# Optimization experiments

Measured on AMD Instinct MI355X. Metric: run time of the kernel, lower is better.

The kernel has to match this reference:

```python
import jax, jax.numpy as jnp
import numpy as np

N_HEADS = 16

def setup_inputs() -> dict:
    key = jax.random.key(0)
    ks = jax.random.split(key, 5)
    d = 2048
    s = 0.02
    return {
        "x": jax.random.normal(ks[0], (1, 2048, d), dtype=jnp.float32),
        "Wq": jax.random.normal(ks[1], (d, d), dtype=jnp.float32) * s,
        "bq": jnp.zeros((d,), jnp.float32),
        "Wk": jax.random.normal(ks[2], (d, d), dtype=jnp.float32) * s,
        "bk": jnp.zeros((d,), jnp.float32),
        "Wv": jax.random.normal(ks[3], (d, d), dtype=jnp.float32) * s,
        "bv": jnp.zeros((d,), jnp.float32),
        "Wo": jax.random.normal(ks[4], (d, d), dtype=jnp.float32) * s,
        "bo": jnp.zeros((d,), jnp.float32),
    }

def reference(x, Wq, bq, Wk, bk, Wv, bv, Wo, bo):
    B, S, D = x.shape
    H = N_HEADS
    dk = D // H
    # QKV projections -> [B, H, S, dk]
    def proj(W, b):
        return (x @ W + b).reshape(B, S, H, dk).transpose(0, 2, 1, 3)
    q, k, v = proj(Wq, bq), proj(Wk, bk), proj(Wv, bv)
    scores = jnp.einsum('bhqd,bhkd->bhqk', q, k) / jnp.sqrt(jnp.float32(dk))
    # _apply_sliding_window_attention: block-reshaped tril == plain causal mask
    causal = jnp.tril(jnp.ones((S, S), dtype=bool))
    scores = jnp.where(causal, scores, -jnp.inf)
    probs = jax.nn.softmax(scores, axis=-1)
    out = jnp.einsum('bhqk,bhkd->bhqd', probs, v)  # [B,H,S,dk]
    out = out.transpose(0, 2, 1, 3).reshape(B, S, D)
    return out @ Wo + bo
```

## Files before the change

### kernel.cpp

```cpp
#include <hip/hip_runtime.h>
#include <hip/hip_bf16.h>
#include <stdint.h>

typedef unsigned short u16;
typedef __attribute__((ext_vector_type(8))) __bf16 bf16x8;
typedef __attribute__((ext_vector_type(4))) float f32x4;

#define LOG2E 1.4426950408889634f

__device__ __forceinline__ float bf2f(u16 u) {
  union { uint32_t u; float f; } v; v.u = ((uint32_t)u) << 16;
  return v.f;
}

__device__ __forceinline__ uint32_t pk2(float a, float b) {
  union { __hip_bfloat162 h; uint32_t u; } x;
  x.h = __float22bfloat162_rn(make_float2(a, b));
  return x.u;
}

__device__ __forceinline__ void gl_lds16(const void* g, void* l) {
  __builtin_amdgcn_global_load_lds((const __attribute__((address_space(1))) void*)g,
                                   (__attribute__((address_space(3))) void*)l,
                                   16, 0, 0);
}

__device__ __forceinline__ f32x4 mfma16(bf16x8 a, bf16x8 b, f32x4 c) {
  return __builtin_amdgcn_mfma_f32_16x16x32_bf16(a, b, c, 0, 0, 0);
}

__global__ void cvt_bf16(const float* __restrict__ src, u16* __restrict__ dst) {
  int i = (blockIdx.x * 256 + threadIdx.x) * 4;
  float4 f = *(const float4*)(src + i);
  uint2 o;
  o.x = pk2(f.x, f.y);
  o.y = pk2(f.z, f.w);
  *(uint2*)(dst + i) = o;
}

__global__ void transpose_cvt(const float* __restrict__ W0, const float* __restrict__ W1,
                              const float* __restrict__ W2, const float* __restrict__ W3,
                              u16* __restrict__ out) {
  __shared__ float tile[64][65];
  int z = blockIdx.z;
  const float* W = (z == 0) ? W0 : (z == 1) ? W1 : (z == 2) ? W2 : W3;
  u16* dst = out + (size_t)z * 2048 * 2048;
  int k0 = blockIdx.y * 64, n0 = blockIdx.x * 64;
  int lx = threadIdx.x & 63, ly = threadIdx.x >> 6;
#pragma unroll
  for (int p = 0; p < 16; ++p) {
    int row = p * 4 + ly;
    tile[row][lx] = W[(size_t)(k0 + row) * 2048 + n0 + lx];
  }
  __syncthreads();
  int kc = threadIdx.x & 7;
  int rbase = threadIdx.x >> 3;
#pragma unroll
  for (int p = 0; p < 2; ++p) {
    int n = rbase + p * 32;
    uint4 o;
    o.x = pk2(tile[kc * 8 + 0][n], tile[kc * 8 + 1][n]);
    o.y = pk2(tile[kc * 8 + 2][n], tile[kc * 8 + 3][n]);
    o.z = pk2(tile[kc * 8 + 4][n], tile[kc * 8 + 5][n]);
    o.w = pk2(tile[kc * 8 + 6][n], tile[kc * 8 + 7][n]);
    *(uint4*)(dst + (size_t)(n0 + n) * 2048 + k0 + kc * 8) = o;
  }
}

__launch_bounds__(256, 2)
__global__ void gemm_bt(const u16* __restrict__ A, const u16* __restrict__ Bt,
                        const float* __restrict__ b0, const float* __restrict__ b1,
                        const float* __restrict__ b2,
                        u16* __restrict__ outQ, u16* __restrict__ outK,
                        u16* __restrict__ outVT) {
  extern __shared__ char smem[];
  u16* As = (u16*)smem;
  u16* Bs = (u16*)(smem + 16384);
  const int K = 2048;
  const int tid = threadIdx.x;
  const int lane = tid & 63, wid = tid >> 6;
  const int c = lane & 15, q = lane >> 4;
  const int wm = wid >> 1, wn = wid & 1;
  const int tm = blockIdx.y, tn = blockIdx.x;
  const size_t Abase = (size_t)tm * 128 * K;
  const size_t Bbase = (size_t)tn * 128 * K;

  f32x4 acc[4][4] = {};

  for (int kt = 0; kt < K / 64; ++kt) {
#pragma unroll
    for (int t = 0; t < 4; ++t) {
      int slot = wid * 256 + t * 64 + lane;
      int row = slot >> 3, cs = slot & 7;
      int cc = cs ^ (row & 7);
      const u16* ga = A + Abase + (size_t)row * K + kt * 64 + cc * 8;
      gl_lds16(ga, (char*)As + (size_t)(wid * 256 + t * 64) * 16);
      const u16* gb = Bt + Bbase + (size_t)row * K + kt * 64 + cc * 8;
      gl_lds16(gb, (char*)Bs + (size_t)(wid * 256 + t * 64) * 16);
    }
    __syncthreads();
#pragma unroll
    for (int kc = 0; kc < 2; ++kc) {
      bf16x8 af[4], bfr[4];
#pragma unroll
      for (int i = 0; i < 4; ++i) {
        int rowa = wm * 64 + i * 16 + c;
        int cha = ((kc << 2) | q) ^ (rowa & 7);
        af[i] = *(const bf16x8*)((const char*)As + rowa * 128 + cha * 16);
        int rowb = wn * 64 + i * 16 + c;
        int chb = ((kc << 2) | q) ^ (rowb & 7);
        bfr[i] = *(const bf16x8*)((const char*)Bs + rowb * 128 + chb * 16);
      }
#pragma unroll
      for (int i = 0; i < 4; ++i)
#pragma unroll
        for (int j = 0; j < 4; ++j)
          acc[i][j] = mfma16(af[i], bfr[j], acc[i][j]);
    }
    __syncthreads();
  }

  int proj = tn >> 4;
  int h = tn & 15;
  const float* bias = (proj == 0) ? b0 : (proj == 1) ? b1 : b2;
  if (proj < 2) {
    u16* out = (proj == 0) ? outQ : outK;
    float scale = (proj == 0) ? 0.08838834764831845f : 1.0f;
#pragma unroll
    for (int i = 0; i < 4; ++i) {
      int s0 = tm * 128 + wm * 64 + i * 16 + q * 4;
#pragma unroll
      for (int j = 0; j < 4; ++j) {
        int d = wn * 64 + j * 16 + c;
        float bv = bias[h * 128 + d];
        uint32_t p01 = pk2((acc[i][j][0] + bv) * scale, (acc[i][j][1] + bv) * scale);
        uint32_t p23 = pk2((acc[i][j][2] + bv) * scale, (acc[i][j][3] + bv) * scale);
        u16* o = out + ((size_t)h * 2048 + s0) * 128 + d;
        o[0]   = (u16)p01;
        o[128] = (u16)(p01 >> 16);
        o[256] = (u16)p23;
        o[384] = (u16)(p23 >> 16);
      }
    }
  } else {
    u16* Cs = (u16*)smem;
#pragma unroll
    for (int i = 0; i < 4; ++i) {
      int sl = wm * 64 + i * 16 + q * 4;
#pragma unroll
      for (int j = 0; j < 4; ++j) {
        int dl = wn * 64 + j * 16 + c;
        float bv = bias[h * 128 + dl];
        uint2 pk;
        pk.x = pk2(acc[i][j][0] + bv, acc[i][j][1] + bv);
        pk.y = pk2(acc[i][j][2] + bv, acc[i][j][3] + bv);
        *(uint2*)(Cs + dl * 136 + sl) = pk;
      }
    }
    __syncthreads();
#pragma unroll
    for (int rr = 0; rr < 8; ++rr) {
      int d = rr * 16 + (tid >> 4);
      int sc = (tid & 15) * 8;
      uint4 vv = *(const uint4*)(Cs + d * 136 + sc);
      *(uint4*)(outVT + ((size_t)(h * 128 + d)) * 2048 + tm * 128 + sc) = vv;
    }
  }
}

__launch_bounds__(256, 2)
__global__ void gemm_op(const u16* __restrict__ A, const u16* __restrict__ Bt,
                        const float* __restrict__ bias, float* __restrict__ out) {
  extern __shared__ char smem[];
  u16* As = (u16*)smem;
  u16* Bs = (u16*)(smem + 16384);
  const int K = 2048;
  const int tid = threadIdx.x;
  const int lane = tid & 63, wid = tid >> 6;
  const int c = lane & 15, q = lane >> 4;
  const int wm = wid >> 1, wn = wid & 1;
  const int tm = blockIdx.y, tn = blockIdx.x;
  const size_t Abase = (size_t)tm * 128 * K;
  const size_t Bbase = (size_t)tn * 64 * K;

  f32x4 acc[4][2] = {};

  for (int kt = 0; kt < K / 64; ++kt) {
#pragma unroll
    for (int t = 0; t < 4; ++t) {
      int slot = wid * 256 + t * 64 + lane;
      int row = slot >> 3, cs = slot & 7;
      int cc = cs ^ (row & 7);
      gl_lds16(A + Abase + (size_t)row * K + kt * 64 + cc * 8,
               (char*)As + (size_t)(wid * 256 + t * 64) * 16);
    }
#pragma unroll
    for (int t = 0; t < 2; ++t) {
      int slot = wid * 128 + t * 64 + lane;
      int row = slot >> 3, cs = slot & 7;
      int cc = cs ^ (row & 7);
      gl_lds16(Bt + Bbase + (size_t)row * K + kt * 64 + cc * 8,
               (char*)Bs + (size_t)(wid * 128 + t * 64) * 16);
    }
    __syncthreads();
#pragma unroll
    for (int kc = 0; kc < 2; ++kc) {
      bf16x8 af[4], bfr[2];
#pragma unroll
      for (int i = 0; i < 4; ++i) {
        int rowa = wm * 64 + i * 16 + c;
        int cha = ((kc << 2) | q) ^ (rowa & 7);
        af[i] = *(const bf16x8*)((const char*)As + rowa * 128 + cha * 16);
      }
#pragma unroll
      for (int j = 0; j < 2; ++j) {
        int rowb = wn * 32 + j * 16 + c;
        int chb = ((kc << 2) | q) ^ (rowb & 7);
        bfr[j] = *(const bf16x8*)((const char*)Bs + rowb * 128 + chb * 16);
      }
#pragma unroll
      for (int i = 0; i < 4; ++i)
#pragma unroll
        for (int j = 0; j < 2; ++j)
          acc[i][j] = mfma16(af[i], bfr[j], acc[i][j]);
    }
    __syncthreads();
  }

#pragma unroll
  for (int i = 0; i < 4; ++i) {
    int rowg = tm * 128 + wm * 64 + i * 16 + q * 4;
#pragma unroll
    for (int j = 0; j < 2; ++j) {
      int colg = tn * 64 + wn * 32 + j * 16 + c;
      float bv = bias[colg];
#pragma unroll
      for (int r = 0; r < 4; ++r)
        out[(size_t)(rowg + r) * 2048 + colg] = acc[i][j][r] + bv;
    }
  }
}

__launch_bounds__(256, 2)
__global__ void attn_kernel(const u16* __restrict__ Qb, const u16* __restrict__ Kb,
                            const u16* __restrict__ Vt,
                            u16* __restrict__ Opb, float* __restrict__ lpb) {
  extern __shared__ char smem[];
  u16* Ks = (u16*)smem;
  u16* Vs = (u16*)(smem + 16384);
  u16* Ps = (u16*)(smem + 32768);
  int b = blockIdx.x;
  int split, qt, h;
  if (b < 256) { split = 0; qt = b >> 4; h = b & 15; }
  else { split = 1; int idx = b - 256; qt = 15 - (idx >> 4); h = idx & 15; }
  u16* Op = Opb + (size_t)split * 4194304;
  float* lp = lpb + (size_t)split * 32768;
  const int ktBase = split ? (qt + 1) : 0;
  const int ntiles = qt + 1;

  const int tid = threadIdx.x, lane = tid & 63, wid = tid >> 6;
  const int c = lane & 15, q = lane >> 4;

  bf16x8 qf[2][4];
#pragma unroll
  for (int i = 0; i < 2; ++i) {
    int s = qt * 128 + wid * 32 + i * 16 + c;
    const u16* qrow = Qb + ((size_t)h * 2048 + s) * 128;
#pragma unroll
    for (int kc = 0; kc < 4; ++kc)
      qf[i][kc] = *(const bf16x8*)(qrow + kc * 32 + q * 8);
  }

  f32x4 oacc[2][8] = {};
  float lst[2][4] = {};

  for (int tt = 0; tt < ntiles; ++tt) {
    const int kt = ktBase + tt;
    if (tt) __syncthreads();
#pragma unroll
    for (int t = 0; t < 4; ++t) {
      int slot = (wid * 4 + t) * 64 + lane;
      int rowk = slot >> 4, csk = slot & 15;
      int cck = csk ^ (rowk & 7);
      const u16* gk = Kb + ((size_t)h * 2048 + kt * 64 + rowk) * 128 + cck * 8;
      gl_lds16(gk, (char*)Ks + (size_t)((wid * 4 + t) * 64) * 16);
      int rowv = slot >> 3, csv = slot & 7;
      int ccv = csv ^ (rowv & 7);
      const u16* gv = Vt + ((size_t)(h * 128 + rowv)) * 2048 + kt * 64 + ccv * 8;
      gl_lds16(gv, (char*)Vs + (size_t)((wid * 4 + t) * 64) * 16);
    }
    __syncthreads();

    f32x4 sacc[2][4] = {};
#pragma unroll
    for (int kc = 0; kc < 4; ++kc) {
      bf16x8 bfr[4];
#pragma unroll
      for (int j = 0; j < 4; ++j) {
        int row = j * 16 + c;
        int ch = ((kc << 2) | q) ^ (row & 7);
        bfr[j] = *(const bf16x8*)((const char*)Ks + row * 256 + ch * 16);
      }
#pragma unroll
      for (int i = 0; i < 2; ++i)
#pragma unroll
        for (int j = 0; j < 4; ++j)
          sacc[i][j] = mfma16(qf[i][kc], bfr[j], sacc[i][j]);
    }

    if (kt >= 2 * qt) {
#pragma unroll
      for (int i = 0; i < 2; ++i)
#pragma unroll
        for (int j = 0; j < 4; ++j) {
          int key = kt * 64 + j * 16 + c;
#pragma unroll
          for (int r = 0; r < 4; ++r) {
            int qrow = qt * 128 + wid * 32 + i * 16 + q * 4 + r;
            if (key > qrow) sacc[i][j][r] = -1e30f;
          }
        }
    }

#pragma unroll
    for (int i = 0; i < 2; ++i)
#pragma unroll
      for (int j = 0; j < 4; ++j)
#pragma unroll
        for (int r = 0; r < 4; ++r) {
          float p = __builtin_amdgcn_exp2f(sacc[i][j][r] * LOG2E);
          sacc[i][j][r] = p;
          lst[i][r] += p;
        }

#pragma unroll
    for (int i = 0; i < 2; ++i)
#pragma unroll
      for (int j = 0; j < 4; ++j) {
        uint32_t p01 = pk2(sacc[i][j][0], sacc[i][j][1]);
        uint32_t p23 = pk2(sacc[i][j][2], sacc[i][j][3]);
        u16* pp = Ps + wid * 2304 + (i * 16 + q * 4) * 72 + j * 16 + c;
        pp[0]   = (u16)p01;
        pp[72]  = (u16)(p01 >> 16);
        pp[144] = (u16)p23;
        pp[216] = (u16)(p23 >> 16);
      }

#pragma unroll
    for (int kc = 0; kc < 2; ++kc) {
      bf16x8 af[2], bv[8];
#pragma unroll
      for (int i = 0; i < 2; ++i)
        af[i] = *(const bf16x8*)((const char*)Ps + wid * 4608 + (i * 16 + c) * 144 +
                                 kc * 64 + q * 16);
#pragma unroll
      for (int jo = 0; jo < 8; ++jo) {
        int row = jo * 16 + c;
        int ch = ((kc << 2) | q) ^ (row & 7);
        bv[jo] = *(const bf16x8*)((const char*)Vs + row * 128 + ch * 16);
      }
#pragma unroll
      for (int i = 0; i < 2; ++i)
#pragma unroll
        for (int jo = 0; jo < 8; ++jo)
          oacc[i][jo] = mfma16(bv[jo], af[i], oacc[i][jo]);
    }
  }

#pragma unroll
  for (int i = 0; i < 2; ++i)
#pragma unroll
    for (int r = 0; r < 4; ++r) {
      float l = lst[i][r];
      l += __shfl_xor(l, 1);
      l += __shfl_xor(l, 2);
      l += __shfl_xor(l, 4);
      l += __shfl_xor(l, 8);
      if (c == 0)
        lp[(size_t)h * 2048 + qt * 128 + wid * 32 + i * 16 + q * 4 + r] = l;
    }
#pragma unroll
  for (int i = 0; i < 2; ++i) {
    int s = qt * 128 + wid * 32 + i * 16 + c;
#pragma unroll
    for (int jo = 0; jo < 8; ++jo) {
      uint2 o;
      o.x = pk2(oacc[i][jo][0], oacc[i][jo][1]);
      o.y = pk2(oacc[i][jo][2], oacc[i][jo][3]);
      *(uint2*)(Op + ((size_t)h * 2048 + s) * 128 + jo * 16 + q * 4) = o;
    }
  }
}

__global__ void attn_combine(const u16* __restrict__ Opb, const float* __restrict__ lpb,
                             u16* __restrict__ AO) {
  int g = blockIdx.x * 256 + threadIdx.x;
  int row = g >> 4;
  int dd = (g & 15) * 8;
  int h = row >> 11, s = row & 2047;
  float inv = 1.0f / (lpb[row] + lpb[row + 32768]);
  uint4 a = *(const uint4*)(Opb + (size_t)row * 128 + dd);
  uint4 bb = *(const uint4*)(Opb + 4194304 + (size_t)row * 128 + dd);
  const u16* pa = (const u16*)&a;
  const u16* pb = (const u16*)&bb;
  uint4 res;
  uint32_t* pr = (uint32_t*)&res;
#pragma unroll
  for (int t = 0; t < 4; ++t)
    pr[t] = pk2((bf2f(pa[2 * t]) + bf2f(pb[2 * t])) * inv,
                (bf2f(pa[2 * t + 1]) + bf2f(pb[2 * t + 1])) * inv);
  *(uint4*)(AO + (size_t)s * 2048 + h * 128 + dd) = res;
}

extern "C" void kernel_launch(void* const* d_in, const int* in_sizes, int n_in,
                              void* d_out, int out_size, void* d_ws, size_t ws_size,
                              hipStream_t stream) {
  const float* x  = (const float*)d_in[0];
  const float* Wq = (const float*)d_in[1];
  const float* bq = (const float*)d_in[2];
  const float* Wk = (const float*)d_in[3];
  const float* bk = (const float*)d_in[4];
  const float* Wv = (const float*)d_in[5];
  const float* bv = (const float*)d_in[6];
  const float* Wo = (const float*)d_in[7];
  const float* bo = (const float*)d_in[8];

  char* ws = (char*)d_ws;
  u16* xb = (u16*)(ws);
  u16* wt = (u16*)(ws + (size_t)8  * 1048576);
  u16* Qb = (u16*)(ws + (size_t)40 * 1048576);
  u16* Kb = (u16*)(ws + (size_t)48 * 1048576);
  u16* Vt = (u16*)(ws + (size_t)56 * 1048576);
  u16* AO = (u16*)(ws + (size_t)64 * 1048576);
  u16* Opb = (u16*)(ws);
  float* lpb = (float*)d_out;

  cvt_bf16<<<4096, 256, 0, stream>>>(x, xb);
  transpose_cvt<<<dim3(32, 32, 4), 256, 0, stream>>>(Wq, Wk, Wv, Wo, wt);
  gemm_bt<<<dim3(48, 16), 256, 34816, stream>>>(xb, wt, bq, bk, bv, Qb, Kb, Vt);
  attn_kernel<<<512, 256, 51200, stream>>>(Qb, Kb, Vt, Opb, lpb);
  attn_combine<<<2048, 256, 0, stream>>>(Opb, lpb, AO);
  gemm_op<<<dim3(32, 16), 256, 24576, stream>>>(AO, wt + (size_t)3 * 2048 * 2048,
                                                bo, (float*)d_out);
}
```

Before: 260.7 us.

## Double-buffer K/V tiles in attention with async prefetch and swizzled P buffer

Measured after the change: 256.9 us. Within noise of the previous version (-1.4%).

```diff
diff --git a/kernel.cpp b/kernel.cpp
--- a/kernel.cpp
+++ b/kernel.cpp
@@ -27,6 +27,12 @@
 
 __device__ __forceinline__ f32x4 mfma16(bf16x8 a, bf16x8 b, f32x4 c) {
   return __builtin_amdgcn_mfma_f32_16x16x32_bf16(a, b, c, 0, 0, 0);
+}
+
+__device__ __forceinline__ void bar() {
+  asm volatile("" ::: "memory");
+  __builtin_amdgcn_s_barrier();
+  asm volatile("" ::: "memory");
 }
 
 __global__ void cvt_bf16(const float* __restrict__ src, u16* __restrict__ dst) {
@@ -246,9 +252,6 @@
                             const u16* __restrict__ Vt,
                             u16* __restrict__ Opb, float* __restrict__ lpb) {
   extern __shared__ char smem[];
-  u16* Ks = (u16*)smem;
-  u16* Vs = (u16*)(smem + 16384);
-  u16* Ps = (u16*)(smem + 32768);
   int b = blockIdx.x;
   int split, qt, h;
   if (b < 256) { split = 0; qt = b >> 4; h = b & 15; }
@@ -274,24 +277,43 @@
   f32x4 oacc[2][8] = {};
   float lst[2][4] = {};
 
-  for (int tt = 0; tt < ntiles; ++tt) {
-    const int kt = ktBase + tt;
-    if (tt) __syncthreads();
+  auto STAGE = [&](int kt, int buf) {
+    char* Kd = smem + buf * 32768;
+    char* Vd = smem + buf * 32768 + 16384;
 #pragma unroll
     for (int t = 0; t < 4; ++t) {
       int slot = (wid * 4 + t) * 64 + lane;
       int rowk = slot >> 4, csk = slot & 15;
       int cck = csk ^ (rowk & 7);
       const u16* gk = Kb + ((size_t)h * 2048 + kt * 64 + rowk) * 128 + cck * 8;
-      gl_lds16(gk, (char*)Ks + (size_t)((wid * 4 + t) * 64) * 16);
+      gl_lds16(gk, Kd + (size_t)((wid * 4 + t) * 64) * 16);
       int rowv = slot >> 3, csv = slot & 7;
       int ccv = csv ^ (rowv & 7);
       const u16* gv = Vt + ((size_t)(h * 128 + rowv)) * 2048 + kt * 64 + ccv * 8;
-      gl_lds16(gv, (char*)Vs + (size_t)((wid * 4 + t) * 64) * 16);
-    }
-    __syncthreads();
+      gl_lds16(gv, Vd + (size_t)((wid * 4 + t) * 64) * 16);
+    }
+  };
+
+  STAGE(ktBase, 0);
+  int cur = 0;
+
+  for (int tt = 0; tt < ntiles; ++tt) {
+    const int kt = ktBase + tt;
+    if (tt + 1 < ntiles) {
+      STAGE(kt + 1, cur ^ 1);
+      __builtin_amdgcn_sched_barrier(0);
+      asm volatile("s_waitcnt vmcnt(8)" ::: "memory");
+    } else {
+      asm volatile("s_waitcnt vmcnt(0)" ::: "memory");
+    }
+    __builtin_amdgcn_sched_barrier(0);
+    bar();
+
+    const char* Ksb = smem + cur * 32768;
+    const char* Vsb = smem + cur * 32768 + 16384;
 
     f32x4 sacc[2][4] = {};
+    __builtin_amdgcn_s_setprio(1);
 #pragma unroll
     for (int kc = 0; kc < 4; ++kc) {
       bf16x8 bfr[4];
@@ -299,7 +321,7 @@
       for (int j = 0; j < 4; ++j) {
         int row = j * 16 + c;
         int ch = ((kc << 2) | q) ^ (row & 7);
-        bfr[j] = *(const bf16x8*)((const char*)Ks + row * 256 + ch * 16);
+        bfr[j] = *(const bf16x8*)(Ksb + row * 256 + ch * 16);
       }
 #pragma unroll
       for (int i = 0; i < 2; ++i)
@@ -307,6 +329,8 @@
         for (int j = 0; j < 4; ++j)
           sacc[i][j] = mfma16(qf[i][kc], bfr[j], sacc[i][j]);
     }
+    __builtin_amdgcn_s_setprio(0);
+    bar();
 
     if (kt >= 2 * qt) {
 #pragma unroll
@@ -333,31 +357,36 @@
           lst[i][r] += p;
         }
 
+    char* Pw = smem + cur * 32768 + wid * 4096;
 #pragma unroll
     for (int i = 0; i < 2; ++i)
 #pragma unroll
       for (int j = 0; j < 4; ++j) {
         uint32_t p01 = pk2(sacc[i][j][0], sacc[i][j][1]);
         uint32_t p23 = pk2(sacc[i][j][2], sacc[i][j][3]);
-        u16* pp = Ps + wid * 2304 + (i * 16 + q * 4) * 72 + j * 16 + c;
-        pp[0]   = (u16)p01;
-        pp[72]  = (u16)(p01 >> 16);
-        pp[144] = (u16)p23;
-        pp[216] = (u16)(p23 >> 16);
-      }
-
+        int cb = (j << 1) | (c >> 3);
+        int r0 = i * 16 + q * 4;
+        int wb = (c & 7) << 1;
+        *(u16*)(Pw + (r0 + 0) * 128 + ((cb ^ ((r0 + 0) & 7)) << 4) + wb) = (u16)p01;
+        *(u16*)(Pw + (r0 + 1) * 128 + ((cb ^ ((r0 + 1) & 7)) << 4) + wb) = (u16)(p01 >> 16);
+        *(u16*)(Pw + (r0 + 2) * 128 + ((cb ^ ((r0 + 2) & 7)) << 4) + wb) = (u16)p23;
+        *(u16*)(Pw + (r0 + 3) * 128 + ((cb ^ ((r0 + 3) & 7)) << 4) + wb) = (u16)(p23 >> 16);
+      }
+
+    __builtin_amdgcn_s_setprio(1);
 #pragma unroll
     for (int kc = 0; kc < 2; ++kc) {
       bf16x8 af[2], bv[8];
 #pragma unroll
-      for (int i = 0; i < 2; ++i)
-        af[i] = *(const bf16x8*)((const char*)Ps + wid * 4608 + (i * 16 + c) * 144 +
-                                 kc * 64 + q * 16);
+      for (int i = 0; i < 2; ++i) {
+        int prow = i * 16 + c;
+        af[i] = *(const bf16x8*)(Pw + prow * 128 + ((((kc << 2) | q) ^ (prow & 7)) << 4));
+      }
 #pragma unroll
       for (int jo = 0; jo < 8; ++jo) {
         int row = jo * 16 + c;
         int ch = ((kc << 2) | q) ^ (row & 7);
-        bv[jo] = *(const bf16x8*)((const char*)Vs + row * 128 + ch * 16);
+        bv[jo] = *(const bf16x8*)(Vsb + row * 128 + ch * 16);
       }
 #pragma unroll
       for (int i = 0; i < 2; ++i)
@@ -365,6 +394,9 @@
         for (int jo = 0; jo < 8; ++jo)
           oacc[i][jo] = mfma16(bv[jo], af[i], oacc[i][jo]);
     }
+    __builtin_amdgcn_s_setprio(0);
+    bar();
+    cur ^= 1;
   }
 
 #pragma unroll
@@ -438,7 +470,7 @@
   cvt_bf16<<<4096, 256, 0, stream>>>(x, xb);
   transpose_cvt<<<dim3(32, 32, 4), 256, 0, stream>>>(Wq, Wk, Wv, Wo, wt);
   gemm_bt<<<dim3(48, 16), 256, 34816, stream>>>(xb, wt, bq, bk, bv, Qb, Kb, Vt);
-  attn_kernel<<<512, 256, 51200, stream>>>(Qb, Kb, Vt, Opb, lpb);
+  attn_kernel<<<512, 256, 65536, stream>>>(Qb, Kb, Vt, Opb, lpb);
   attn_combine<<<2048, 256, 0, stream>>>(Opb, lpb, AO);
   gemm_op<<<dim3(32, 16), 256, 24576, stream>>>(AO, wt + (size_t)3 * 2048 * 2048,
                                                 bo, (float*)d_out);
```
